# Kernel tuning notes

Hardware: AMD Instinct MI355X
Metric: run time of the kernel (lower is better)

## Reference

```python
import jax, jax.numpy as jnp
import numpy as np

N_NODES = 50000
N_EDGES = 400000
IN_DIM = 128
HID_DIM = 128
OUT_DIM = 128


def setup_inputs() -> dict:
    key = jax.random.key(0)
    k_x, k_e, k_w1, k_b1, k_w2, k_b2 = jax.random.split(key, 6)
    x = jax.random.normal(k_x, (N_NODES, IN_DIM), dtype=jnp.float32)
    edge_index = jax.random.randint(k_e, (2, N_EDGES), 0, N_NODES, dtype=jnp.int64)
    # nn.Linear-style params: W is [out, in], kaiming-uniform-ish init
    lim1 = 1.0 / np.sqrt(IN_DIM)
    lim2 = 1.0 / np.sqrt(HID_DIM)
    W1 = jax.random.uniform(k_w1, (HID_DIM, IN_DIM), jnp.float32, -lim1, lim1)
    b1 = jax.random.uniform(k_b1, (HID_DIM,), jnp.float32, -lim1, lim1)
    W2 = jax.random.uniform(k_w2, (OUT_DIM, HID_DIM), jnp.float32, -lim2, lim2)
    b2 = jax.random.uniform(k_b2, (OUT_DIM,), jnp.float32, -lim2, lim2)
    return {"x": x, "edge_index": edge_index, "W1": W1, "b1": b1, "W2": W2, "b2": b2}


def reference(x, edge_index, W1, b1, W2, b2):
    # h = relu(fc1(x));  dropout in eval mode -> identity
    h = jax.nn.relu(x @ W1.T + b1)                      # [N, hid]
    src, dst = edge_index[0], edge_index[1]
    # gather messages from src, scatter-add (mean) into dst
    agg = jax.ops.segment_sum(h[src], dst, num_segments=N_NODES)      # [N, hid]
    deg = jax.ops.segment_sum(jnp.ones_like(dst, dtype=h.dtype), dst,
                              num_segments=N_NODES)                   # [N]
    deg = jnp.maximum(deg, 1.0)
    agg = agg / deg[:, None]
    # residual add + fc2
    return (agg + h) @ W2.T + b2                        # [N, out]
```

## Files before the change

### kernel.cpp

```cpp
#include <hip/hip_runtime.h>

#define N_NODES 50000
#define N_EDGES 400000
#define DIM 128
#define CNT_BLK ((N_EDGES + 2047) / 2048)
#define FC1_BLK ((N_NODES + 63) / 64)
#define AGG_BLK ((N_NODES + 31) / 32)
#define SLOTS 96

typedef unsigned short u16;
typedef unsigned int   u32;
typedef __bf16 v8bf  __attribute__((ext_vector_type(8)));
typedef float  f32x4 __attribute__((ext_vector_type(4)));
typedef u16    u16x8 __attribute__((ext_vector_type(8)));

union BF8 { u16x8 u; v8bf b; };

__device__ __forceinline__ float bf2f(u16 u) {
    union { u32 i; float f; } v; v.i = ((u32)u) << 16; return v.f;
}
__device__ __forceinline__ u16 f2bf(float f) {
    union { float f; u32 i; } v; v.f = f; u32 u = v.i;
    return (u16)((u + 0x7FFFu + ((u >> 16) & 1u)) >> 16);
}

__global__ __launch_bounds__(256, 3) void build_fc1_kernel(
    const int* __restrict__ esrc, const int* __restrict__ edst,
    int* __restrict__ counts, int* __restrict__ esorted,
    const float* __restrict__ W2, u16* __restrict__ Wb2,
    const float* __restrict__ x, const float* __restrict__ W1,
    const float* __restrict__ b1, u16* __restrict__ h)
{
    __shared__ u16 xs[64 * 136];
    const int bid = blockIdx.x;

    if (bid < CNT_BLK) {
        int e0 = bid * 2048 + threadIdx.x * 8;
        if (e0 + 8 <= N_EDGES) {
            int4 da = *(const int4*)(edst + e0);
            int4 db = *(const int4*)(edst + e0 + 4);
            int4 sa = *(const int4*)(esrc + e0);
            int4 sb = *(const int4*)(esrc + e0 + 4);
            int o0 = atomicAdd(&counts[da.x], 1);
            int o1 = atomicAdd(&counts[da.y], 1);
            int o2 = atomicAdd(&counts[da.z], 1);
            int o3 = atomicAdd(&counts[da.w], 1);
            int o4 = atomicAdd(&counts[db.x], 1);
            int o5 = atomicAdd(&counts[db.y], 1);
            int o6 = atomicAdd(&counts[db.z], 1);
            int o7 = atomicAdd(&counts[db.w], 1);
            if (o0 < SLOTS) esorted[da.x * SLOTS + o0] = sa.x;
            if (o1 < SLOTS) esorted[da.y * SLOTS + o1] = sa.y;
            if (o2 < SLOTS) esorted[da.z * SLOTS + o2] = sa.z;
            if (o3 < SLOTS) esorted[da.w * SLOTS + o3] = sa.w;
            if (o4 < SLOTS) esorted[db.x * SLOTS + o4] = sb.x;
            if (o5 < SLOTS) esorted[db.y * SLOTS + o5] = sb.y;
            if (o6 < SLOTS) esorted[db.z * SLOTS + o6] = sb.z;
            if (o7 < SLOTS) esorted[db.w * SLOTS + o7] = sb.w;
        } else if (e0 < N_EDGES) {
            for (int j = 0; j < 8 && e0 + j < N_EDGES; ++j) {
                int d = edst[e0 + j], s = esrc[e0 + j];
                if ((unsigned)d < N_NODES && (unsigned)s < N_NODES) {
                    int o = atomicAdd(&counts[d], 1);
                    if (o < SLOTS) esorted[d * SLOTS + o] = s;
                }
            }
        }
        return;
    }
    if (bid < CNT_BLK + 64) {
        int i = (bid - CNT_BLK) * 256 + threadIdx.x;
        Wb2[i] = f2bf(W2[i]);
        return;
    }
    if (bid == CNT_BLK + 64) {
        if (threadIdx.x < 128)
            *(u32*)(h + (size_t)N_NODES * DIM + threadIdx.x * 2) = 0u;
        return;
    }

    const int t = threadIdx.x;
    const int wave = t >> 6, lane = t & 63, quad = lane >> 4, l15 = lane & 15;
    const int ch = wave >> 1, rh = wave & 1;
    const int row0 = (bid - (CNT_BLK + 65)) * 64;

    BF8 barr[4][4];
#pragma unroll
    for (int ct = 0; ct < 4; ++ct)
#pragma unroll
        for (int ks = 0; ks < 4; ++ks) {
            const float* wp = W1 + (size_t)(ch * 64 + ct * 16 + l15) * DIM
                                 + ks * 32 + quad * 8;
            float4 f0 = *(const float4*)wp;
            float4 f1 = *(const float4*)(wp + 4);
            u16x8 p;
            p[0] = f2bf(f0.x); p[1] = f2bf(f0.y); p[2] = f2bf(f0.z); p[3] = f2bf(f0.w);
            p[4] = f2bf(f1.x); p[5] = f2bf(f1.y); p[6] = f2bf(f1.z); p[7] = f2bf(f1.w);
            barr[ct][ks].u = p;
        }

    {
        int srow = t >> 2, k0 = (t & 3) * 32;
        int grow = row0 + srow; if (grow >= N_NODES) grow = N_NODES - 1;
        const float* xp = x + (size_t)grow * DIM + k0;
#pragma unroll
        for (int j = 0; j < 4; ++j) {
            float4 f0 = *(const float4*)(xp + j * 8);
            float4 f1 = *(const float4*)(xp + j * 8 + 4);
            u16x8 p;
            p[0] = f2bf(f0.x); p[1] = f2bf(f0.y); p[2] = f2bf(f0.z); p[3] = f2bf(f0.w);
            p[4] = f2bf(f1.x); p[5] = f2bf(f1.y); p[6] = f2bf(f1.z); p[7] = f2bf(f1.w);
            *(u16x8*)&xs[srow * 136 + k0 + j * 8] = p;
        }
    }

    f32x4 acc[2][4];
#pragma unroll
    for (int ct = 0; ct < 4; ++ct) {
        float bv = b1[ch * 64 + ct * 16 + l15];
        acc[0][ct] = (f32x4){bv, bv, bv, bv};
        acc[1][ct] = (f32x4){bv, bv, bv, bv};
    }
    __syncthreads();

#pragma unroll
    for (int ks = 0; ks < 4; ++ks) {
        BF8 a0, a1;
        a0.u = *(const u16x8*)&xs[(rh * 32 +  0 + l15) * 136 + ks * 32 + quad * 8];
        a1.u = *(const u16x8*)&xs[(rh * 32 + 16 + l15) * 136 + ks * 32 + quad * 8];
#pragma unroll
        for (int ct = 0; ct < 4; ++ct) {
            acc[0][ct] = __builtin_amdgcn_mfma_f32_16x16x32_bf16(
                a0.b, barr[ct][ks].b, acc[0][ct], 0, 0, 0);
            acc[1][ct] = __builtin_amdgcn_mfma_f32_16x16x32_bf16(
                a1.b, barr[ct][ks].b, acc[1][ct], 0, 0, 0);
        }
    }

#pragma unroll
    for (int rt = 0; rt < 2; ++rt)
#pragma unroll
        for (int i = 0; i < 4; ++i) {
            int row = row0 + rh * 32 + rt * 16 + quad * 4 + i;
            if (row < N_NODES) {
#pragma unroll
                for (int ct = 0; ct < 4; ++ct) {
                    int col = ch * 64 + ct * 16 + l15;
                    h[(size_t)row * DIM + col] = f2bf(fmaxf(acc[rt][ct][i], 0.f));
                }
            }
        }
}

__global__ __launch_bounds__(256, 6) void agg_fc2_kernel(
    const int* __restrict__ counts, const int* __restrict__ esorted,
    const u16* __restrict__ h, const u16* __restrict__ Wb2,
    const float* __restrict__ b2, float* __restrict__ out)
{
    __shared__ u16 xs[32 * 136];
    const int t = threadIdx.x;
    const int wv = t >> 6, lane = t & 63, quad = lane >> 4, l15 = lane & 15;
    const int row0 = blockIdx.x * 32;

    {
        const int s0 = wv * 8 + quad * 2;
        const int n0 = row0 + s0;
        const int n1 = n0 + 1;
        const bool va = (n0 < N_NODES), vb = (n1 < N_NODES);
        int deg0 = 0, deg1 = 0;
        if (va) deg0 = counts[n0];
        if (vb) deg1 = counts[n1];
        const int degc0 = (deg0 < SLOTS) ? deg0 : SLOTS;
        const int degc1 = (deg1 < SLOTS) ? deg1 : SLOTS;
        const int f0 = degc0 & ~3;
        const int f1 = degc1 & ~3;

        u16x8 hres0 = (u16x8){0,0,0,0,0,0,0,0};
        u16x8 hres1 = (u16x8){0,0,0,0,0,0,0,0};
        if (va) hres0 = *(const u16x8*)(h + (size_t)n0 * DIM + l15 * 8);
        if (vb) hres1 = *(const u16x8*)(h + (size_t)n1 * DIM + l15 * 8);

        float a0[8], a1[8];
#pragma unroll
        for (int j = 0; j < 8; ++j) { a0[j] = 0.f; a1[j] = 0.f; }

        const int* ep0 = esorted + (size_t)n0 * SLOTS;
        const int* ep1 = esorted + (size_t)n1 * SLOTS;
        int k0 = 0, k1 = 0;

        if (k0 < f0 && k1 < f1) {
            int4 ia = *(const int4*)(ep0);
            int4 ib = *(const int4*)(ep1);
            while (true) {
                u16x8 v0 = *(const u16x8*)(h + (size_t)ia.x * DIM + l15 * 8);
                u16x8 v1 = *(const u16x8*)(h + (size_t)ia.y * DIM + l15 * 8);
                u16x8 v2 = *(const u16x8*)(h + (size_t)ia.z * DIM + l15 * 8);
                u16x8 v3 = *(const u16x8*)(h + (size_t)ia.w * DIM + l15 * 8);
                u16x8 w0 = *(const u16x8*)(h + (size_t)ib.x * DIM + l15 * 8);
                u16x8 w1 = *(const u16x8*)(h + (size_t)ib.y * DIM + l15 * 8);
                u16x8 w2 = *(const u16x8*)(h + (size_t)ib.z * DIM + l15 * 8);
                u16x8 w3 = *(const u16x8*)(h + (size_t)ib.w * DIM + l15 * 8);
                k0 += 4; k1 += 4;
                const bool more = (k0 < f0) & (k1 < f1);
                int4 ian, ibn;
                if (more) {
                    ian = *(const int4*)(ep0 + k0);
                    ibn = *(const int4*)(ep1 + k1);
                }
#pragma unroll
                for (int j = 0; j < 8; ++j) {
                    a0[j] += bf2f(v0[j]); a0[j] += bf2f(v1[j]);
                    a0[j] += bf2f(v2[j]); a0[j] += bf2f(v3[j]);
                    a1[j] += bf2f(w0[j]); a1[j] += bf2f(w1[j]);
                    a1[j] += bf2f(w2[j]); a1[j] += bf2f(w3[j]);
                }
                if (!more) break;
                ia = ian; ib = ibn;
            }
        }
        while (k0 < f0) {
            int4 ia = *(const int4*)(ep0 + k0);
            u16x8 v0 = *(const u16x8*)(h + (size_t)ia.x * DIM + l15 * 8);
            u16x8 v1 = *(const u16x8*)(h + (size_t)ia.y * DIM + l15 * 8);
            u16x8 v2 = *(const u16x8*)(h + (size_t)ia.z * DIM + l15 * 8);
            u16x8 v3 = *(const u16x8*)(h + (size_t)ia.w * DIM + l15 * 8);
#pragma unroll
            for (int j = 0; j < 8; ++j) {
                a0[j] += bf2f(v0[j]); a0[j] += bf2f(v1[j]);
                a0[j] += bf2f(v2[j]); a0[j] += bf2f(v3[j]);
            }
            k0 += 4;
        }
        if (k0 < degc0) {
            int4 ia = *(const int4*)(ep0 + k0);
            ia.x = (k0 + 0 < degc0) ? ia.x : N_NODES;
            ia.y = (k0 + 1 < degc0) ? ia.y : N_NODES;
            ia.z = (k0 + 2 < degc0) ? ia.z : N_NODES;
            ia.w = N_NODES;
            u16x8 v0 = *(const u16x8*)(h + (size_t)ia.x * DIM + l15 * 8);
            u16x8 v1 = *(const u16x8*)(h + (size_t)ia.y * DIM + l15 * 8);
            u16x8 v2 = *(const u16x8*)(h + (size_t)ia.z * DIM + l15 * 8);
            u16x8 v3 = *(const u16x8*)(h + (size_t)ia.w * DIM + l15 * 8);
#pragma unroll
            for (int j = 0; j < 8; ++j) {
                a0[j] += bf2f(v0[j]); a0[j] += bf2f(v1[j]);
                a0[j] += bf2f(v2[j]); a0[j] += bf2f(v3[j]);
            }
        }
        while (k1 < f1) {
            int4 ia = *(const int4*)(ep1 + k1);
            u16x8 v0 = *(const u16x8*)(h + (size_t)ia.x * DIM + l15 * 8);
            u16x8 v1 = *(const u16x8*)(h + (size_t)ia.y * DIM + l15 * 8);
            u16x8 v2 = *(const u16x8*)(h + (size_t)ia.z * DIM + l15 * 8);
            u16x8 v3 = *(const u16x8*)(h + (size_t)ia.w * DIM + l15 * 8);
#pragma unroll
            for (int j = 0; j < 8; ++j) {
                a1[j] += bf2f(v0[j]); a1[j] += bf2f(v1[j]);
                a1[j] += bf2f(v2[j]); a1[j] += bf2f(v3[j]);
            }
            k1 += 4;
        }
        if (k1 < degc1) {
            int4 ia = *(const int4*)(ep1 + k1);
            ia.x = (k1 + 0 < degc1) ? ia.x : N_NODES;
            ia.y = (k1 + 1 < degc1) ? ia.y : N_NODES;
            ia.z = (k1 + 2 < degc1) ? ia.z : N_NODES;
            ia.w = N_NODES;
            u16x8 v0 = *(const u16x8*)(h + (size_t)ia.x * DIM + l15 * 8);
            u16x8 v1 = *(const u16x8*)(h + (size_t)ia.y * DIM + l15 * 8);
            u16x8 v2 = *(const u16x8*)(h + (size_t)ia.z * DIM + l15 * 8);
            u16x8 v3 = *(const u16x8*)(h + (size_t)ia.w * DIM + l15 * 8);
#pragma unroll
            for (int j = 0; j < 8; ++j) {
                a1[j] += bf2f(v0[j]); a1[j] += bf2f(v1[j]);
                a1[j] += bf2f(v2[j]); a1[j] += bf2f(v3[j]);
            }
        }

        float inv0 = (deg0 > 0) ? 1.f / (float)deg0 : 1.f;
        float inv1 = (deg1 > 0) ? 1.f / (float)deg1 : 1.f;
        u16x8 pk0, pk1;
#pragma unroll
        for (int j = 0; j < 8; ++j) {
            pk0[j] = f2bf(a0[j] * inv0 + bf2f(hres0[j]));
            pk1[j] = f2bf(a1[j] * inv1 + bf2f(hres1[j]));
        }
        *(u16x8*)&xs[s0 * 136 + l15 * 8]       = pk0;
        *(u16x8*)&xs[(s0 + 1) * 136 + l15 * 8] = pk1;
    }

    BF8 barr[2][4];
#pragma unroll
    for (int ct = 0; ct < 2; ++ct)
#pragma unroll
        for (int ks = 0; ks < 4; ++ks)
            barr[ct][ks].u = *(const u16x8*)(
                Wb2 + (size_t)(wv * 32 + ct * 16 + l15) * DIM + ks * 32 + quad * 8);

    f32x4 acc[2][2];
#pragma unroll
    for (int ct = 0; ct < 2; ++ct) {
        float bv = b2[wv * 32 + ct * 16 + l15];
        acc[0][ct] = (f32x4){bv, bv, bv, bv};
        acc[1][ct] = (f32x4){bv, bv, bv, bv};
    }
    __syncthreads();

#pragma unroll
    for (int ks = 0; ks < 4; ++ks) {
        BF8 A0, A1;
        A0.u = *(const u16x8*)&xs[( 0 + l15) * 136 + ks * 32 + quad * 8];
        A1.u = *(const u16x8*)&xs[(16 + l15) * 136 + ks * 32 + quad * 8];
#pragma unroll
        for (int ct = 0; ct < 2; ++ct) {
            acc[0][ct] = __builtin_amdgcn_mfma_f32_16x16x32_bf16(
                A0.b, barr[ct][ks].b, acc[0][ct], 0, 0, 0);
            acc[1][ct] = __builtin_amdgcn_mfma_f32_16x16x32_bf16(
                A1.b, barr[ct][ks].b, acc[1][ct], 0, 0, 0);
        }
    }

#pragma unroll
    for (int rt = 0; rt < 2; ++rt)
#pragma unroll
        for (int i = 0; i < 4; ++i) {
            int row = row0 + rt * 16 + quad * 4 + i;
            if (row < N_NODES) {
#pragma unroll
                for (int ct = 0; ct < 2; ++ct) {
                    int col = wv * 32 + ct * 16 + l15;
                    out[(size_t)row * DIM + col] = acc[rt][ct][i];
                }
            }
        }
}

extern "C" void kernel_launch(void* const* d_in, const int* in_sizes, int n_in,
                              void* d_out, int out_size, void* d_ws, size_t ws_size,
                              hipStream_t stream)
{
    const float* x  = (const float*)d_in[0];
    const int*   ei = (const int*)d_in[1];
    const float* W1 = (const float*)d_in[2];
    const float* b1 = (const float*)d_in[3];
    const float* W2 = (const float*)d_in[4];
    const float* b2 = (const float*)d_in[5];
    float* out = (float*)d_out;

    const int* esrc = ei;
    const int* edst = ei + N_EDGES;

    char* ws = (char*)d_ws;
    size_t off = 0;
    u16* h       = (u16*)(ws + off); off += (size_t)(N_NODES + 1) * DIM * 2;
    u16* Wb2     = (u16*)(ws + off); off += (size_t)DIM * DIM * 2;
    int* counts  = (int*)(ws + off); off += (size_t)N_NODES * 4;
    int* esorted = (int*)(ws + off); off += (size_t)N_NODES * SLOTS * 4;

    hipMemsetAsync(counts, 0, (size_t)N_NODES * 4, stream);

    build_fc1_kernel<<<CNT_BLK + 65 + FC1_BLK, 256, 0, stream>>>(
        esrc, edst, counts, esorted, W2, Wb2, x, W1, b1, h);
    agg_fc2_kernel<<<AGG_BLK, 256, 0, stream>>>(
        counts, esorted, h, Wb2, b2, out);
}
```

Measured before the change: 154.7 us.

## Apply fc2 before aggregation using linearity, aggregate projected features

Uses the linearity of fc2 to compute y = h·W2ᵀ per node right after fc1 in the first kernel, then aggregates y over neighbours and adds the residual and bias in the second kernel. This removes the MFMA, shared-memory staging and W2 conversion from the gather kernel, so the gather kernel writes its output directly. It adds a second GEMM and an extra register tile to the fc1 kernel. The y rows are rounded to bf16 before aggregation, which changes where rounding happens.

```diff
diff --git a/kernel.cpp b/kernel.cpp
--- a/kernel.cpp
+++ b/kernel.cpp
@@ -24,12 +24,12 @@
     return (u16)((u + 0x7FFFu + ((u >> 16) & 1u)) >> 16);
 }
 
-__global__ __launch_bounds__(256, 3) void build_fc1_kernel(
+__global__ __launch_bounds__(256, 3) void build_fc12_kernel(
     const int* __restrict__ esrc, const int* __restrict__ edst,
     int* __restrict__ counts, int* __restrict__ esorted,
-    const float* __restrict__ W2, u16* __restrict__ Wb2,
-    const float* __restrict__ x, const float* __restrict__ W1,
-    const float* __restrict__ b1, u16* __restrict__ h)
+    const float* __restrict__ x,
+    const float* __restrict__ W1, const float* __restrict__ b1,
+    const float* __restrict__ W2, u16* __restrict__ y)
 {
     __shared__ u16 xs[64 * 136];
     const int bid = blockIdx.x;
@@ -68,21 +68,16 @@
         }
         return;
     }
-    if (bid < CNT_BLK + 64) {
-        int i = (bid - CNT_BLK) * 256 + threadIdx.x;
-        Wb2[i] = f2bf(W2[i]);
-        return;
-    }
-    if (bid == CNT_BLK + 64) {
-        if (threadIdx.x < 128)
-            *(u32*)(h + (size_t)N_NODES * DIM + threadIdx.x * 2) = 0u;
+    if (bid == CNT_BLK) {
+        if (threadIdx.x < 64)
+            ((u32*)(y + (size_t)N_NODES * DIM))[threadIdx.x] = 0u;
         return;
     }
 
     const int t = threadIdx.x;
     const int wave = t >> 6, lane = t & 63, quad = lane >> 4, l15 = lane & 15;
     const int ch = wave >> 1, rh = wave & 1;
-    const int row0 = (bid - (CNT_BLK + 65)) * 64;
+    const int row0 = (bid - (CNT_BLK + 1)) * 64;
 
     BF8 barr[4][4];
 #pragma unroll
@@ -136,6 +131,55 @@
                 a1.b, barr[ct][ks].b, acc[1][ct], 0, 0, 0);
         }
     }
+    __syncthreads();
+
+#pragma unroll
+    for (int rt = 0; rt < 2; ++rt)
+#pragma unroll
+        for (int i = 0; i < 4; ++i) {
+            int rl = rh * 32 + rt * 16 + quad * 4 + i;
+#pragma unroll
+            for (int ct = 0; ct < 4; ++ct)
+                xs[rl * 136 + ch * 64 + ct * 16 + l15] =
+                    f2bf(fmaxf(acc[rt][ct][i], 0.f));
+        }
+
+    BF8 barr2[4][4];
+#pragma unroll
+    for (int ct = 0; ct < 4; ++ct)
+#pragma unroll
+        for (int ks = 0; ks < 4; ++ks) {
+            const float* wp = W2 + (size_t)(ch * 64 + ct * 16 + l15) * DIM
+                                 + ks * 32 + quad * 8;
+            float4 f0 = *(const float4*)wp;
+            float4 f1 = *(const float4*)(wp + 4);
+            u16x8 p;
+            p[0] = f2bf(f0.x); p[1] = f2bf(f0.y); p[2] = f2bf(f0.z); p[3] = f2bf(f0.w);
+            p[4] = f2bf(f1.x); p[5] = f2bf(f1.y); p[6] = f2bf(f1.z); p[7] = f2bf(f1.w);
+            barr2[ct][ks].u = p;
+        }
+
+    f32x4 acc2[2][4];
+#pragma unroll
+    for (int ct = 0; ct < 4; ++ct) {
+        acc2[0][ct] = (f32x4){0.f, 0.f, 0.f, 0.f};
+        acc2[1][ct] = (f32x4){0.f, 0.f, 0.f, 0.f};
+    }
+    __syncthreads();
+
+#pragma unroll
+    for (int ks = 0; ks < 4; ++ks) {
+        BF8 a0, a1;
+        a0.u = *(const u16x8*)&xs[(rh * 32 +  0 + l15) * 136 + ks * 32 + quad * 8];
+        a1.u = *(const u16x8*)&xs[(rh * 32 + 16 + l15) * 136 + ks * 32 + quad * 8];
+#pragma unroll
+        for (int ct = 0; ct < 4; ++ct) {
+            acc2[0][ct] = __builtin_amdgcn_mfma_f32_16x16x32_bf16(
+                a0.b, barr2[ct][ks].b, acc2[0][ct], 0, 0, 0);
+            acc2[1][ct] = __builtin_amdgcn_mfma_f32_16x16x32_bf16(
+                a1.b, barr2[ct][ks].b, acc2[1][ct], 0, 0, 0);
+        }
+    }
 
 #pragma unroll
     for (int rt = 0; rt < 2; ++rt)
@@ -146,193 +190,166 @@
 #pragma unroll
                 for (int ct = 0; ct < 4; ++ct) {
                     int col = ch * 64 + ct * 16 + l15;
-                    h[(size_t)row * DIM + col] = f2bf(fmaxf(acc[rt][ct][i], 0.f));
+                    y[(size_t)row * DIM + col] = f2bf(acc2[rt][ct][i]);
                 }
             }
         }
 }
 
-__global__ __launch_bounds__(256, 6) void agg_fc2_kernel(
+__global__ __launch_bounds__(256, 6) void agg_out_kernel(
     const int* __restrict__ counts, const int* __restrict__ esorted,
-    const u16* __restrict__ h, const u16* __restrict__ Wb2,
-    const float* __restrict__ b2, float* __restrict__ out)
+    const u16* __restrict__ y, const float* __restrict__ b2,
+    float* __restrict__ out)
 {
-    __shared__ u16 xs[32 * 136];
     const int t = threadIdx.x;
     const int wv = t >> 6, lane = t & 63, quad = lane >> 4, l15 = lane & 15;
     const int row0 = blockIdx.x * 32;
 
-    {
-        const int s0 = wv * 8 + quad * 2;
-        const int n0 = row0 + s0;
-        const int n1 = n0 + 1;
-        const bool va = (n0 < N_NODES), vb = (n1 < N_NODES);
-        int deg0 = 0, deg1 = 0;
-        if (va) deg0 = counts[n0];
-        if (vb) deg1 = counts[n1];
-        const int degc0 = (deg0 < SLOTS) ? deg0 : SLOTS;
-        const int degc1 = (deg1 < SLOTS) ? deg1 : SLOTS;
-        const int f0 = degc0 & ~3;
-        const int f1 = degc1 & ~3;
-
-        u16x8 hres0 = (u16x8){0,0,0,0,0,0,0,0};
-        u16x8 hres1 = (u16x8){0,0,0,0,0,0,0,0};
-        if (va) hres0 = *(const u16x8*)(h + (size_t)n0 * DIM + l15 * 8);
-        if (vb) hres1 = *(const u16x8*)(h + (size_t)n1 * DIM + l15 * 8);
-
-        float a0[8], a1[8];
-#pragma unroll
-        for (int j = 0; j < 8; ++j) { a0[j] = 0.f; a1[j] = 0.f; }
-
-        const int* ep0 = esorted + (size_t)n0 * SLOTS;
-        const int* ep1 = esorted + (size_t)n1 * SLOTS;
-        int k0 = 0, k1 = 0;
-
-        if (k0 < f0 && k1 < f1) {
-            int4 ia = *(const int4*)(ep0);
-            int4 ib = *(const int4*)(ep1);
-            while (true) {
-                u16x8 v0 = *(const u16x8*)(h + (size_t)ia.x * DIM + l15 * 8);
-                u16x8 v1 = *(const u16x8*)(h + (size_t)ia.y * DIM + l15 * 8);
-                u16x8 v2 = *(const u16x8*)(h + (size_t)ia.z * DIM + l15 * 8);
-                u16x8 v3 = *(const u16x8*)(h + (size_t)ia.w * DIM + l15 * 8);
-                u16x8 w0 = *(const u16x8*)(h + (size_t)ib.x * DIM + l15 * 8);
-                u16x8 w1 = *(const u16x8*)(h + (size_t)ib.y * DIM + l15 * 8);
-                u16x8 w2 = *(const u16x8*)(h + (size_t)ib.z * DIM + l15 * 8);
-                u16x8 w3 = *(const u16x8*)(h + (size_t)ib.w * DIM + l15 * 8);
-                k0 += 4; k1 += 4;
-                const bool more = (k0 < f0) & (k1 < f1);
-                int4 ian, ibn;
-                if (more) {
-                    ian = *(const int4*)(ep0 + k0);
-                    ibn = *(const int4*)(ep1 + k1);
-                }
-#pragma unroll
-                for (int j = 0; j < 8; ++j) {
-                    a0[j] += bf2f(v0[j]); a0[j] += bf2f(v1[j]);
-                    a0[j] += bf2f(v2[j]); a0[j] += bf2f(v3[j]);
-                    a1[j] += bf2f(w0[j]); a1[j] += bf2f(w1[j]);
-                    a1[j] += bf2f(w2[j]); a1[j] += bf2f(w3[j]);
-                }
-                if (!more) break;
-                ia = ian; ib = ibn;
+    const int s0 = wv * 8 + quad * 2;
+    const int n0 = row0 + s0;
+    const int n1 = n0 + 1;
+    const bool va = (n0 < N_NODES), vb = (n1 < N_NODES);
+    int deg0 = 0, deg1 = 0;
+    if (va) deg0 = counts[n0];
+    if (vb) deg1 = counts[n1];
+    const int degc0 = (deg0 < SLOTS) ? deg0 : SLOTS;
+    const int degc1 = (deg1 < SLOTS) ? deg1 : SLOTS;
+    const int f0 = degc0 & ~3;
+    const int f1 = degc1 & ~3;
+
+    u16x8 yres0 = (u16x8){0,0,0,0,0,0,0,0};
+    u16x8 yres1 = (u16x8){0,0,0,0,0,0,0,0};
+    if (va) yres0 = *(const u16x8*)(y + (size_t)n0 * DIM + l15 * 8);
+    if (vb) yres1 = *(const u16x8*)(y + (size_t)n1 * DIM + l15 * 8);
+
+    float a0[8], a1[8];
+#pragma unroll
+    for (int j = 0; j < 8; ++j) { a0[j] = 0.f; a1[j] = 0.f; }
+
+    const int* ep0 = esorted + (size_t)n0 * SLOTS;
+    const int* ep1 = esorted + (size_t)n1 * SLOTS;
+    int k0 = 0, k1 = 0;
+
+    if (k0 < f0 && k1 < f1) {
+        int4 ia = *(const int4*)(ep0);
+        int4 ib = *(const int4*)(ep1);
+        while (true) {
+            u16x8 v0 = *(const u16x8*)(y + (size_t)ia.x * DIM + l15 * 8);
+            u16x8 v1 = *(const u16x8*)(y + (size_t)ia.y * DIM + l15 * 8);
+            u16x8 v2 = *(const u16x8*)(y + (size_t)ia.z * DIM + l15 * 8);
+            u16x8 v3 = *(const u16x8*)(y + (size_t)ia.w * DIM + l15 * 8);
+            u16x8 w0 = *(const u16x8*)(y + (size_t)ib.x * DIM + l15 * 8);
+            u16x8 w1 = *(const u16x8*)(y + (size_t)ib.y * DIM + l15 * 8);
+            u16x8 w2 = *(const u16x8*)(y + (size_t)ib.z * DIM + l15 * 8);
+            u16x8 w3 = *(const u16x8*)(y + (size_t)ib.w * DIM + l15 * 8);
+            k0 += 4; k1 += 4;
+            const bool more = (k0 < f0) & (k1 < f1);
+            int4 ian, ibn;
+            if (more) {
+                ian = *(const int4*)(ep0 + k0);
+                ibn = *(const int4*)(ep1 + k1);
             }
-        }
-        while (k0 < f0) {
-            int4 ia = *(const int4*)(ep0 + k0);
-            u16x8 v0 = *(const u16x8*)(h + (size_t)ia.x * DIM + l15 * 8);
-            u16x8 v1 = *(const u16x8*)(h + (size_t)ia.y * DIM + l15 * 8);
-            u16x8 v2 = *(const u16x8*)(h + (size_t)ia.z * DIM + l15 * 8);
-            u16x8 v3 = *(const u16x8*)(h + (size_t)ia.w * DIM + l15 * 8);
 #pragma unroll
             for (int j = 0; j < 8; ++j) {
                 a0[j] += bf2f(v0[j]); a0[j] += bf2f(v1[j]);
                 a0[j] += bf2f(v2[j]); a0[j] += bf2f(v3[j]);
+                a1[j] += bf2f(w0[j]); a1[j] += bf2f(w1[j]);
+                a1[j] += bf2f(w2[j]); a1[j] += bf2f(w3[j]);
             }
-            k0 += 4;
-        }
-        if (k0 < degc0) {
-            int4 ia = *(const int4*)(ep0 + k0);
-            ia.x = (k0 + 0 < degc0) ? ia.x : N_NODES;
-            ia.y = (k0 + 1 < degc0) ? ia.y : N_NODES;
-            ia.z = (k0 + 2 < degc0) ? ia.z : N_NODES;
-            ia.w = N_NODES;
-            u16x8 v0 = *(const u16x8*)(h + (size_t)ia.x * DIM + l15 * 8);
-            u16x8 v1 = *(const u16x8*)(h + (size_t)ia.y * DIM + l15 * 8);
-            u16x8 v2 = *(const u16x8*)(h + (size_t)ia.z * DIM + l15 * 8);
-            u16x8 v3 = *(const u16x8*)(h + (size_t)ia.w * DIM + l15 * 8);
-#pragma unroll
-            for (int j = 0; j < 8; ++j) {
-                a0[j] += bf2f(v0[j]); a0[j] += bf2f(v1[j]);
-                a0[j] += bf2f(v2[j]); a0[j] += bf2f(v3[j]);
-            }
-        }
-        while (k1 < f1) {
-            int4 ia = *(const int4*)(ep1 + k1);
-            u16x8 v0 = *(const u16x8*)(h + (size_t)ia.x * DIM + l15 * 8);
-            u16x8 v1 = *(const u16x8*)(h + (size_t)ia.y * DIM + l15 * 8);
-            u16x8 v2 = *(const u16x8*)(h + (size_t)ia.z * DIM + l15 * 8);
-            u16x8 v3 = *(const u16x8*)(h + (size_t)ia.w * DIM + l15 * 8);
-#pragma unroll
-            for (int j = 0; j < 8; ++j) {
-                a1[j] += bf2f(v0[j]); a1[j] += bf2f(v1[j]);
-                a1[j] += bf2f(v2[j]); a1[j] += bf2f(v3[j]);
-            }
-            k1 += 4;
-        }
-        if (k1 < degc1) {
-            int4 ia = *(const int4*)(ep1 + k1);
-            ia.x = (k1 + 0 < degc1) ? ia.x : N_NODES;
-            ia.y = (k1 + 1 < degc1) ? ia.y : N_NODES;
-            ia.z = (k1 + 2 < degc1) ? ia.z : N_NODES;
-            ia.w = N_NODES;
-            u16x8 v0 = *(const u16x8*)(h + (size_t)ia.x * DIM + l15 * 8);
-            u16x8 v1 = *(const u16x8*)(h + (size_t)ia.y * DIM + l15 * 8);
-            u16x8 v2 = *(const u16x8*)(h + (size_t)ia.z * DIM + l15 * 8);
-            u16x8 v3 = *(const u16x8*)(h + (size_t)ia.w * DIM + l15 * 8);
-#pragma unroll
-            for (int j = 0; j < 8; ++j) {
-                a1[j] += bf2f(v0[j]); a1[j] += bf2f(v1[j]);
-                a1[j] += bf2f(v2[j]); a1[j] += bf2f(v3[j]);
-            }
-        }
-
-        float inv0 = (deg0 > 0) ? 1.f / (float)deg0 : 1.f;
-        float inv1 = (deg1 > 0) ? 1.f / (float)deg1 : 1.f;
-        u16x8 pk0, pk1;
+            if (!more) break;
+            ia = ian; ib = ibn;
+        }
+    }
+    while (k0 < f0) {
+        int4 ia = *(const int4*)(ep0 + k0);
+        u16x8 v0 = *(const u16x8*)(y + (size_t)ia.x * DIM + l15 * 8);
+        u16x8 v1 = *(const u16x8*)(y + (size_t)ia.y * DIM + l15 * 8);
+        u16x8 v2 = *(const u16x8*)(y + (size_t)ia.z * DIM + l15 * 8);
+        u16x8 v3 = *(const u16x8*)(y + (size_t)ia.w * DIM + l15 * 8);
 #pragma unroll
         for (int j = 0; j < 8; ++j) {
-            pk0[j] = f2bf(a0[j] * inv0 + bf2f(hres0[j]));
-            pk1[j] = f2bf(a1[j] * inv1 + bf2f(hres1[j]));
-        }
-        *(u16x8*)&xs[s0 * 136 + l15 * 8]       = pk0;
-        *(u16x8*)&xs[(s0 + 1) * 136 + l15 * 8] = pk1;
-    }
-
-    BF8 barr[2][4];
-#pragma unroll
-    for (int ct = 0; ct < 2; ++ct)
-#pragma unroll
-        for (int ks = 0; ks < 4; ++ks)
-            barr[ct][ks].u = *(const u16x8*)(
-                Wb2 + (size_t)(wv * 32 + ct * 16 + l15) * DIM + ks * 32 + quad * 8);
-
-    f32x4 acc[2][2];
-#pragma unroll
-    for (int ct = 0; ct < 2; ++ct) {
-        float bv = b2[wv * 32 + ct * 16 + l15];
-        acc[0][ct] = (f32x4){bv, bv, bv, bv};
-        acc[1][ct] = (f32x4){bv, bv, bv, bv};
-    }
-    __syncthreads();
-
-#pragma unroll
-    for (int ks = 0; ks < 4; ++ks) {
-        BF8 A0, A1;
-        A0.u = *(const u16x8*)&xs[( 0 + l15) * 136 + ks * 32 + quad * 8];
-        A1.u = *(const u16x8*)&xs[(16 + l15) * 136 + ks * 32 + quad * 8];
-#pragma unroll
-        for (int ct = 0; ct < 2; ++ct) {
-            acc[0][ct] = __builtin_amdgcn_mfma_f32_16x16x32_bf16(
-                A0.b, barr[ct][ks].b, acc[0][ct], 0, 0, 0);
-            acc[1][ct] = __builtin_amdgcn_mfma_f32_16x16x32_bf16(
-                A1.b, barr[ct][ks].b, acc[1][ct], 0, 0, 0);
-        }
-    }
-
-#pragma unroll
-    for (int rt = 0; rt < 2; ++rt)
-#pragma unroll
-        for (int i = 0; i < 4; ++i) {
-            int row = row0 + rt * 16 + quad * 4 + i;
-            if (row < N_NODES) {
-#pragma unroll
-                for (int ct = 0; ct < 2; ++ct) {
-                    int col = wv * 32 + ct * 16 + l15;
-                    out[(size_t)row * DIM + col] = acc[rt][ct][i];
-                }
-            }
-        }
+            a0[j] += bf2f(v0[j]); a0[j] += bf2f(v1[j]);
+            a0[j] += bf2f(v2[j]); a0[j] += bf2f(v3[j]);
+        }
+        k0 += 4;
+    }
+    if (k0 < degc0) {
+        int4 ia = *(const int4*)(ep0 + k0);
+        ia.x = (k0 + 0 < degc0) ? ia.x : N_NODES;
+        ia.y = (k0 + 1 < degc0) ? ia.y : N_NODES;
+        ia.z = (k0 + 2 < degc0) ? ia.z : N_NODES;
+        ia.w = N_NODES;
+        u16x8 v0 = *(const u16x8*)(y + (size_t)ia.x * DIM + l15 * 8);
+        u16x8 v1 = *(const u16x8*)(y + (size_t)ia.y * DIM + l15 * 8);
+        u16x8 v2 = *(const u16x8*)(y + (size_t)ia.z * DIM + l15 * 8);
+        u16x8 v3 = *(const u16x8*)(y + (size_t)ia.w * DIM + l15 * 8);
+#pragma unroll
+        for (int j = 0; j < 8; ++j) {
+            a0[j] += bf2f(v0[j]); a0[j] += bf2f(v1[j]);
+            a0[j] += bf2f(v2[j]); a0[j] += bf2f(v3[j]);
+        }
+    }
+    while (k1 < f1) {
+        int4 ia = *(const int4*)(ep1 + k1);
+        u16x8 v0 = *(const u16x8*)(y + (size_t)ia.x * DIM + l15 * 8);
+        u16x8 v1 = *(const u16x8*)(y + (size_t)ia.y * DIM + l15 * 8);
+        u16x8 v2 = *(const u16x8*)(y + (size_t)ia.z * DIM + l15 * 8);
+        u16x8 v3 = *(const u16x8*)(y + (size_t)ia.w * DIM + l15 * 8);
+#pragma unroll
+        for (int j = 0; j < 8; ++j) {
+            a1[j] += bf2f(v0[j]); a1[j] += bf2f(v1[j]);
+            a1[j] += bf2f(v2[j]); a1[j] += bf2f(v3[j]);
+        }
+        k1 += 4;
+    }
+    if (k1 < degc1) {
+        int4 ia = *(const int4*)(ep1 + k1);
+        ia.x = (k1 + 0 < degc1) ? ia.x : N_NODES;
+        ia.y = (k1 + 1 < degc1) ? ia.y : N_NODES;
+        ia.z = (k1 + 2 < degc1) ? ia.z : N_NODES;
+        ia.w = N_NODES;
+        u16x8 v0 = *(const u16x8*)(y + (size_t)ia.x * DIM + l15 * 8);
+        u16x8 v1 = *(const u16x8*)(y + (size_t)ia.y * DIM + l15 * 8);
+        u16x8 v2 = *(const u16x8*)(y + (size_t)ia.z * DIM + l15 * 8);
+        u16x8 v3 = *(const u16x8*)(y + (size_t)ia.w * DIM + l15 * 8);
+#pragma unroll
+        for (int j = 0; j < 8; ++j) {
+            a1[j] += bf2f(v0[j]); a1[j] += bf2f(v1[j]);
+            a1[j] += bf2f(v2[j]); a1[j] += bf2f(v3[j]);
+        }
+    }
+
+    float4 bA = *(const float4*)(b2 + l15 * 8);
+    float4 bB = *(const float4*)(b2 + l15 * 8 + 4);
+    float inv0 = (deg0 > 0) ? 1.f / (float)deg0 : 1.f;
+    float inv1 = (deg1 > 0) ? 1.f / (float)deg1 : 1.f;
+
+    if (va) {
+        float4 oA, oB;
+        oA.x = a0[0] * inv0 + bf2f(yres0[0]) + bA.x;
+        oA.y = a0[1] * inv0 + bf2f(yres0[1]) + bA.y;
+        oA.z = a0[2] * inv0 + bf2f(yres0[2]) + bA.z;
+        oA.w = a0[3] * inv0 + bf2f(yres0[3]) + bA.w;
+        oB.x = a0[4] * inv0 + bf2f(yres0[4]) + bB.x;
+        oB.y = a0[5] * inv0 + bf2f(yres0[5]) + bB.y;
+        oB.z = a0[6] * inv0 + bf2f(yres0[6]) + bB.z;
+        oB.w = a0[7] * inv0 + bf2f(yres0[7]) + bB.w;
+        *(float4*)(out + (size_t)n0 * DIM + l15 * 8)     = oA;
+        *(float4*)(out + (size_t)n0 * DIM + l15 * 8 + 4) = oB;
+    }
+    if (vb) {
+        float4 oA, oB;
+        oA.x = a1[0] * inv1 + bf2f(yres1[0]) + bA.x;
+        oA.y = a1[1] * inv1 + bf2f(yres1[1]) + bA.y;
+        oA.z = a1[2] * inv1 + bf2f(yres1[2]) + bA.z;
+        oA.w = a1[3] * inv1 + bf2f(yres1[3]) + bA.w;
+        oB.x = a1[4] * inv1 + bf2f(yres1[4]) + bB.x;
+        oB.y = a1[5] * inv1 + bf2f(yres1[5]) + bB.y;
+        oB.z = a1[6] * inv1 + bf2f(yres1[6]) + bB.z;
+        oB.w = a1[7] * inv1 + bf2f(yres1[7]) + bB.w;
+        *(float4*)(out + (size_t)n1 * DIM + l15 * 8)     = oA;
+        *(float4*)(out + (size_t)n1 * DIM + l15 * 8 + 4) = oB;
+    }
 }
 
 extern "C" void kernel_launch(void* const* d_in, const int* in_sizes, int n_in,
@@ -352,15 +369,14 @@
 
     char* ws = (char*)d_ws;
     size_t off = 0;
-    u16* h       = (u16*)(ws + off); off += (size_t)(N_NODES + 1) * DIM * 2;
-    u16* Wb2     = (u16*)(ws + off); off += (size_t)DIM * DIM * 2;
+    u16* y       = (u16*)(ws + off); off += (size_t)(N_NODES + 1) * DIM * 2;
     int* counts  = (int*)(ws + off); off += (size_t)N_NODES * 4;
     int* esorted = (int*)(ws + off); off += (size_t)N_NODES * SLOTS * 4;
 
     hipMemsetAsync(counts, 0, (size_t)N_NODES * 4, stream);
 
-    build_fc1_kernel<<<CNT_BLK + 65 + FC1_BLK, 256, 0, stream>>>(
-        esrc, edst, counts, esorted, W2, Wb2, x, W1, b1, h);
-    agg_fc2_kernel<<<AGG_BLK, 256, 0, stream>>>(
-        counts, esorted, h, Wb2, b2, out);
-}
+    build_fc12_kernel<<<CNT_BLK + 1 + FC1_BLK, 256, 0, stream>>>(
+        esrc, edst, counts, esorted, x, W1, b1, W2, y);
+    agg_out_kernel<<<AGG_BLK, 256, 0, stream>>>(
+        counts, esorted, y, b2, out);
+}
```

Measured after the change: 161.1 us. 1.04x slower.
